# Performance work log

Hardware: AMD Instinct MI355X
Metric: run time of the kernel (lower is better)

Reference implementation:

```python
import jax, jax.numpy as jnp
import numpy as np

B, T, E = 4, 2048, 1024
H, D = 8, 128  # num_query_heads, head_dimension (single shared KV head -> MQA)


def sinusoidal_pe(length, dim, dtype=jnp.float32):
    """Standard additive sinusoidal PE table of shape (length, dim)."""
    pos = jnp.arange(length, dtype=jnp.float32)[:, None]            # (L, 1)
    inv_freq = jnp.exp(-jnp.log(jnp.float32(10000.0)) * (jnp.arange(0, dim, 2, dtype=jnp.float32) / dim))
    ang = pos * inv_freq[None, :]                                    # (L, dim//2)
    pe = jnp.zeros((length, dim), dtype=jnp.float32)
    pe = pe.at[:, 0::2].set(jnp.sin(ang)).at[:, 1::2].set(jnp.cos(ang))
    return pe.astype(dtype)


def setup_inputs() -> dict:
    key = jax.random.key(0)
    kx, kq, kk, kv, ko = jax.random.split(key, 5)
    s = 0.02  # weight init scale
    return {
        "x": jax.random.normal(kx, (B, T, E), dtype=jnp.float32),
        "Wq": jax.random.normal(kq, (H * D, E), dtype=jnp.float32) * s,
        "Wk": jax.random.normal(kk, (D, E), dtype=jnp.float32) * s,
        "Wv": jax.random.normal(kv, (D, E), dtype=jnp.float32) * s,
        "Wo": jax.random.normal(ko, (E, H * D), dtype=jnp.float32) * s,
    }


def reference(x, Wq, Wk, Wv, Wo):
    Bv, Tv, Ev = x.shape
    scale = 1.0 / jnp.sqrt(jnp.float32(D)).astype(x.dtype)

    q = (x @ Wq.T).reshape(Bv, Tv, H, D)        # (B, T, H, D)
    k = (x @ Wk.T).reshape(Bv, Tv, 1, D)        # (B, T, 1, D) single KV head
    v = (x @ Wv.T).reshape(Bv, Tv, 1, D)

    # positional_embedding applied along axis -2 (as in (.., seq, dim) layout):
    # for k (B,T,1,D) the -2 axis has length 1 -> adds pe[0];
    # for q after permute (B,H,T,D) the -2 axis is T -> full table.
    k = k + sinusoidal_pe(1, D, k.dtype)        # broadcast over (B, T)

    q = jnp.transpose(q, (0, 2, 1, 3))          # (B, H, T, D)
    k1 = k[:, :, 0, :]                          # (B, T, D) shared KV head
    v1 = v[:, :, 0, :]                          # (B, T, D)

    q = q + sinusoidal_pe(Tv, D, q.dtype)[None, None]

    # MQA SDPA: broadcast single K/V head across H query heads
    scores = jnp.einsum("bhtd,bsd->bhts", q, k1) * scale   # (B, H, T, T)
    causal = jnp.tril(jnp.ones((Tv, Tv), dtype=bool))
    scores = jnp.where(causal[None, None], scores, jnp.finfo(scores.dtype).min)
    probs = jax.nn.softmax(scores, axis=-1)
    attn = jnp.einsum("bhts,bsd->bhtd", probs, v1)          # (B, H, T, D)

    out = jnp.transpose(attn, (0, 2, 1, 3)).reshape(Bv, Tv, H * D)
    return out @ Wo.T                                        # (B, T, E)
```

## Files before the change

kernel.cpp:

```cpp
#include <hip/hip_runtime.h>
#include <hip/hip_bf16.h>
#include <cstdint>
#include <cstddef>

#define B_ 4
#define T_ 2048
#define E_ 1024
#define H_ 8
#define D_ 128

typedef unsigned short u16;
typedef __bf16 bf16x8 __attribute__((ext_vector_type(8)));
typedef float f32x4 __attribute__((ext_vector_type(4)));

#define MFMA16(a, b, c) __builtin_amdgcn_mfma_f32_16x16x32_bf16((a), (b), (c), 0, 0, 0)

#if defined(__has_builtin)
#if __has_builtin(__builtin_amdgcn_global_load_lds)
#define HAVE_GLL 1
#endif
#endif

__device__ __forceinline__ void gload_lds16(const u16* g, u16* l) {
#ifdef HAVE_GLL
  __builtin_amdgcn_global_load_lds(
      (const __attribute__((address_space(1))) void*)g,
      (__attribute__((address_space(3))) void*)l, 16, 0, 0);
#else
  int lane = threadIdx.x & 63;
  *(uint4*)(l + lane * 8) = *(const uint4*)(g);
#endif
}

__device__ __forceinline__ u16 f2bf(float f) {
  union { float f; uint32_t u; } a; a.f = f;
  uint32_t u = a.u;
  uint32_t r = (u + 0x7fffu + ((u >> 16) & 1u)) >> 16;
  return (u16)r;
}

__device__ __forceinline__ uint32_t pkbf(float lo, float hi) {
  uint32_t r;
  asm volatile("v_cvt_pk_bf16_f32 %0, %1, %2" : "=v"(r) : "v"(lo), "v"(hi));
  return r;
}

__device__ __forceinline__ void cvt4(const float* __restrict__ s, u16* __restrict__ d, int i4) {
  float4 v = *(const float4*)(s + (size_t)i4 * 4);
  uint2 o;
  o.x = (uint32_t)f2bf(v.x) | ((uint32_t)f2bf(v.y) << 16);
  o.y = (uint32_t)f2bf(v.z) | ((uint32_t)f2bf(v.w) << 16);
  *(uint2*)(d + (size_t)i4 * 4) = o;
}

__global__ __launch_bounds__(256) void prep_kernel(
    const float* __restrict__ x,  const float* __restrict__ Wq,
    const float* __restrict__ Wk, const float* __restrict__ Wv,
    const float* __restrict__ Wo,
    u16* __restrict__ xbf, u16* __restrict__ Wcat, u16* __restrict__ Wobf,
    float* __restrict__ pe)
{
  int id = blockIdx.x * 256 + threadIdx.x;
  if (id < 2097152) { cvt4(x, xbf, id); return; }
  id -= 2097152;
  if (id < 262144) { cvt4(Wq, Wcat, id); return; }
  id -= 262144;
  if (id < 32768) { cvt4(Wk, Wcat + 1048576, id); return; }
  id -= 32768;
  if (id < 32768) { cvt4(Wv, Wcat + 1179648, id); return; }
  id -= 32768;
  if (id < 262144) { cvt4(Wo, Wobf, id); return; }
  id -= 262144;
  int t = id >> 6, i = id & 63;
  float f = expf(-logf(10000.0f) * (float)i / 64.0f);
  float ang = (float)t * f;
  pe[t * 128 + 2 * i]     = sinf(ang);
  pe[t * 128 + 2 * i + 1] = cosf(ang);
}

template<int MODE>
__global__ __launch_bounds__(256) void gemm_nt(
    const u16* __restrict__ A, const u16* __restrict__ Bm,
    u16* __restrict__ Qb, u16* __restrict__ Kb, u16* __restrict__ VTb,
    const float* __restrict__ pe, float* __restrict__ Cout, int K)
{
  __shared__ u16 Al[128 * 32];
  __shared__ u16 Bl[128 * 32];
  const int t = threadIdx.x;
  const int l = t & 63, w = t >> 6;
  const int wr = w >> 1, wc = w & 1;
  const int bm = blockIdx.x * 128, bn = blockIdx.y * 128;
  const int lr = l & 15, lg = l >> 4;

  const int srow = w * 32 + (l >> 2);
  const int scol = (l & 3) * 8;
  const u16* gA0 = A + (size_t)(bm + srow) * K + scol;
  const u16* gB0 = Bm + (size_t)(bn + srow) * K + scol;
  u16* lA0 = &Al[(w * 32) * 32];
  u16* lA1 = &Al[(w * 32 + 16) * 32];
  u16* lB0 = &Bl[(w * 32) * 32];
  u16* lB1 = &Bl[(w * 32 + 16) * 32];
  const size_t r16 = (size_t)16 * K;

  f32x4 acc[4][4] = {};

  for (int k0 = 0; k0 < K; k0 += 32) {
    gload_lds16(gA0 + k0, lA0);
    gload_lds16(gA0 + r16 + k0, lA1);
    gload_lds16(gB0 + k0, lB0);
    gload_lds16(gB0 + r16 + k0, lB1);
    __syncthreads();
    bf16x8 af[4], bfr[4];
    #pragma unroll
    for (int m = 0; m < 4; ++m)
      af[m] = *(const bf16x8*)(&Al[(wr * 64 + m * 16 + lr) * 32 + lg * 8]);
    #pragma unroll
    for (int n = 0; n < 4; ++n)
      bfr[n] = *(const bf16x8*)(&Bl[(wc * 64 + n * 16 + lr) * 32 + lg * 8]);
    __builtin_amdgcn_s_setprio(1);
    #pragma unroll
    for (int m = 0; m < 4; ++m) {
      #pragma unroll
      for (int n = 0; n < 4; ++n)
        acc[m][n] = MFMA16(af[m], bfr[n], acc[m][n]);
    }
    __builtin_amdgcn_s_setprio(0);
    __syncthreads();
  }

  const float qscale = 0.08838834764831845f;
  #pragma unroll
  for (int m = 0; m < 4; ++m) {
    #pragma unroll
    for (int n = 0; n < 4; ++n) {
      const int gm0 = bm + wr * 64 + m * 16 + lg * 4;
      const int gn = bn + wc * 64 + n * 16 + lr;
      if constexpr (MODE == 0) {
        const int b = gm0 >> 11, tq0 = gm0 & (T_ - 1);
        if (gn < 1024) {
          int hh = gn >> 7, d = gn & 127;
          #pragma unroll
          for (int r = 0; r < 4; ++r)
            Qb[(((size_t)(b * H_ + hh) * T_ + tq0 + r) << 7) + d] =
                f2bf((acc[m][n][r] + pe[((tq0 + r) << 7) + d]) * qscale);
        } else if (gn < 1152) {
          int d = gn - 1024;
          #pragma unroll
          for (int r = 0; r < 4; ++r)
            Kb[((size_t)(gm0 + r) << 7) + d] = f2bf(acc[m][n][r] + (float)(d & 1));
        } else {
          int d = gn - 1152;
          uint2 pk;
          pk.x = pkbf(acc[m][n][0], acc[m][n][1]);
          pk.y = pkbf(acc[m][n][2], acc[m][n][3]);
          *(uint2*)(VTb + ((size_t)(b * 128 + d) << 11) + tq0) = pk;
        }
      } else {
        #pragma unroll
        for (int r = 0; r < 4; ++r)
          Cout[(size_t)(gm0 + r) * 1024 + gn] = acc[m][n][r];
      }
    }
  }
}

__global__ __launch_bounds__(512) void attn_kernel(
    const u16* __restrict__ Qb, const u16* __restrict__ Kb,
    const u16* __restrict__ VTg, u16* __restrict__ Ob)
{
  __shared__ u16 Kl[128 * 136];
  __shared__ u16 VTl[128 * 136];
  __shared__ u16 Pl[8 * 16 * 136];
  const int t = threadIdx.x;
  const int l = t & 63, w = t >> 6;
  const int lr = l & 15, lg = l >> 4;
  const int p = blockIdx.x, b = blockIdx.y;
  const int h = w;
  const int q0A = p * 16, q0B = (127 - p) * 16;
  const int ntA = (q0A + 16 + 127) >> 7, ntB = (q0B + 16 + 127) >> 7;

  const u16* qbA = Qb + (((size_t)(b * H_ + h) * T_ + q0A + lr) << 7);
  const u16* qbB = Qb + (((size_t)(b * H_ + h) * T_ + q0B + lr) << 7);
  bf16x8 qfA[4], qfB[4];
  #pragma unroll
  for (int kc = 0; kc < 4; ++kc) {
    qfA[kc] = *(const bf16x8*)(qbA + kc * 32 + lg * 8);
    qfB[kc] = *(const bf16x8*)(qbB + kc * 32 + lg * 8);
  }

  float mA = -3e38f, mB = -3e38f, lA = 0.f, lB = 0.f;
  f32x4 oA[8] = {}, oB[8] = {};
  u16* pw = &Pl[w * 16 * 136];

  auto process = [&](f32x4 (&s)[8], float& m, float& lsum, f32x4 (&o)[8],
                     int q0F, int kt, bool masked) {
    float pv[32];
    float pm = -3e38f;
    if (masked) {
      const int qv = q0F + lr;
      #pragma unroll
      for (int kvf = 0; kvf < 8; ++kvf) {
        #pragma unroll
        for (int r = 0; r < 4; ++r) {
          int kv = kt * 128 + kvf * 16 + lg * 4 + r;
          float sv = (kv <= qv) ? s[kvf][r] : -3e38f;
          pv[kvf * 4 + r] = sv;
          pm = fmaxf(pm, sv);
        }
      }
    } else {
      #pragma unroll
      for (int kvf = 0; kvf < 8; ++kvf) {
        #pragma unroll
        for (int r = 0; r < 4; ++r) {
          float sv = s[kvf][r];
          pv[kvf * 4 + r] = sv;
          pm = fmaxf(pm, sv);
        }
      }
    }
    pm = fmaxf(pm, __shfl_xor(pm, 16));
    pm = fmaxf(pm, __shfl_xor(pm, 32));
    float mn;
    if (__all(pm <= m + 8.0f)) {
      mn = m;
    } else {
      mn = fmaxf(m, pm);
      float corr = __expf(m - mn);
      lsum *= corr;
      #pragma unroll
      for (int df = 0; df < 8; ++df) {
        #pragma unroll
        for (int r = 0; r < 4; ++r) o[df][r] *= corr;
      }
      m = mn;
    }
    float ps = 0.f;
    #pragma unroll
    for (int i = 0; i < 32; ++i) {
      pv[i] = __expf(pv[i] - mn);
      ps += pv[i];
    }
    ps += __shfl_xor(ps, 16);
    ps += __shfl_xor(ps, 32);
    lsum += ps;
    #pragma unroll
    for (int kvf = 0; kvf < 8; ++kvf) {
      uint2 pk;
      pk.x = pkbf(pv[kvf * 4 + 0], pv[kvf * 4 + 1]);
      pk.y = pkbf(pv[kvf * 4 + 2], pv[kvf * 4 + 3]);
      *(uint2*)(&pw[lr * 136 + kvf * 16 + lg * 4]) = pk;
    }
    __builtin_amdgcn_s_setprio(1);
    #pragma unroll
    for (int kc = 0; kc < 4; ++kc) {
      bf16x8 pf = *(const bf16x8*)(&pw[lr * 136 + kc * 32 + lg * 8]);
      #pragma unroll
      for (int df = 0; df < 8; ++df) {
        bf16x8 vf = *(const bf16x8*)(&VTl[(df * 16 + lr) * 136 + kc * 32 + lg * 8]);
        o[df] = MFMA16(vf, pf, o[df]);
      }
    }
    __builtin_amdgcn_s_setprio(0);
  };

  for (int kt = 0; kt < ntB; ++kt) {
    #pragma unroll
    for (int it = 0; it < 4; ++it) {
      int cc = it * 512 + t;
      int row = cc >> 4, u = cc & 15;
      *(uint4*)(&Kl[row * 136 + u * 8]) =
          *(const uint4*)(Kb + ((size_t)(b * T_ + kt * 128 + row) << 7) + u * 8);
      *(uint4*)(&VTl[row * 136 + u * 8]) =
          *(const uint4*)(VTg + ((size_t)(b * 128 + row) << 11) + kt * 128 + u * 8);
    }
    __syncthreads();

    const bool actA = kt < ntA;
    f32x4 sA[8] = {}, sB[8] = {};
    __builtin_amdgcn_s_setprio(1);
    #pragma unroll
    for (int kvf = 0; kvf < 8; ++kvf) {
      bf16x8 kf[4];
      #pragma unroll
      for (int kc = 0; kc < 4; ++kc)
        kf[kc] = *(const bf16x8*)(&Kl[(kvf * 16 + lr) * 136 + kc * 32 + lg * 8]);
      #pragma unroll
      for (int kc = 0; kc < 4; ++kc)
        sB[kvf] = MFMA16(kf[kc], qfB[kc], sB[kvf]);
      if (actA) {
        #pragma unroll
        for (int kc = 0; kc < 4; ++kc)
          sA[kvf] = MFMA16(kf[kc], qfA[kc], sA[kvf]);
      }
    }
    __builtin_amdgcn_s_setprio(0);
    process(sB, mB, lB, oB, q0B, kt, kt * 128 + 127 > q0B);
    if (actA) process(sA, mA, lA, oA, q0A, kt, kt * 128 + 127 > q0A);
    __syncthreads();
  }

  float rA = 1.0f / lA, rB = 1.0f / lB;
  #pragma unroll
  for (int df = 0; df < 8; ++df) {
    uint2 pk;
    pk.x = pkbf(oB[df][0] * rB, oB[df][1] * rB);
    pk.y = pkbf(oB[df][2] * rB, oB[df][3] * rB);
    *(uint2*)(Ob + ((size_t)(b * T_ + q0B + lr) << 10) + h * 128 + df * 16 + lg * 4) = pk;
    pk.x = pkbf(oA[df][0] * rA, oA[df][1] * rA);
    pk.y = pkbf(oA[df][2] * rA, oA[df][3] * rA);
    *(uint2*)(Ob + ((size_t)(b * T_ + q0A + lr) << 10) + h * 128 + df * 16 + lg * 4) = pk;
  }
}

extern "C" void kernel_launch(void* const* d_in, const int* in_sizes, int n_in,
                              void* d_out, int out_size, void* d_ws, size_t ws_size,
                              hipStream_t stream) {
  const float* x  = (const float*)d_in[0];
  const float* Wq = (const float*)d_in[1];
  const float* Wk = (const float*)d_in[2];
  const float* Wv = (const float*)d_in[3];
  const float* Wo = (const float*)d_in[4];

  char* ws = (char*)d_ws;
  size_t off = 0;
  auto alloc = [&](size_t bytes) {
    char* p = ws + off;
    off += (bytes + 255) & ~(size_t)255;
    return p;
  };
  u16*   xbf  = (u16*)  alloc(8388608ull * 2);
  u16*   Wcat = (u16*)  alloc(1310720ull * 2);
  u16*   Wobf = (u16*)  alloc(1048576ull * 2);
  float* pe   = (float*)alloc(262144ull * 4);
  u16*   Qbuf = (u16*)  alloc(8388608ull * 2);
  u16*   Kbuf = (u16*)  alloc(1048576ull * 2);
  u16*   VTbuf= (u16*)  alloc(1048576ull * 2);
  u16*   Abuf = (u16*)  alloc(8388608ull * 2);

  prep_kernel<<<11008, 256, 0, stream>>>(x, Wq, Wk, Wv, Wo, xbf, Wcat, Wobf, pe);

  gemm_nt<0><<<dim3(64, 10), 256, 0, stream>>>(xbf, Wcat, Qbuf, Kbuf, VTbuf, pe, nullptr, 1024);
  attn_kernel<<<dim3(64, 4), 512, 0, stream>>>(Qbuf, Kbuf, VTbuf, Abuf);
  gemm_nt<1><<<dim3(64, 8), 256, 0, stream>>>(Abuf, Wobf, nullptr, nullptr, nullptr, nullptr,
                                              (float*)d_out, 1024);
}
```

Baseline: 153.5 us.

## Interleave softmax for both query tiles, use exp2 with log2e-folded scale

The two query tiles (A and B) handled by each wave now share one softmax and PV pass: separate P buffers in LDS let the max, exp and sum steps for both tiles interleave. The PV loop loads each V fragment once and feeds it to both accumulators. The Q scale now includes log2(e), so exp2f replaces __expf and the rescale threshold becomes 11.5 in base 2. This cuts redundant V loads from LDS and gives the scheduler more independent work, at the cost of more LDS and higher register pressure.

```diff
diff --git a/kernel.cpp b/kernel.cpp
--- a/kernel.cpp
+++ b/kernel.cpp
@@ -2,6 +2,7 @@
 #include <hip/hip_bf16.h>
 #include <cstdint>
 #include <cstddef>
+#include <cmath>
 
 #define B_ 4
 #define T_ 2048
@@ -128,7 +129,7 @@
     __syncthreads();
   }
 
-  const float qscale = 0.08838834764831845f;
+  const float qscale = 0.12752869468f;
   #pragma unroll
   for (int m = 0; m < 4; ++m) {
     #pragma unroll
@@ -170,7 +171,8 @@
 {
   __shared__ u16 Kl[128 * 136];
   __shared__ u16 VTl[128 * 136];
-  __shared__ u16 Pl[8 * 16 * 136];
+  __shared__ u16 PlB[8 * 16 * 136];
+  __shared__ u16 PlA[8 * 16 * 136];
   const int t = threadIdx.x;
   const int l = t & 63, w = t >> 6;
   const int lr = l & 15, lg = l >> 4;
@@ -190,79 +192,8 @@
 
   float mA = -3e38f, mB = -3e38f, lA = 0.f, lB = 0.f;
   f32x4 oA[8] = {}, oB[8] = {};
-  u16* pw = &Pl[w * 16 * 136];
-
-  auto process = [&](f32x4 (&s)[8], float& m, float& lsum, f32x4 (&o)[8],
-                     int q0F, int kt, bool masked) {
-    float pv[32];
-    float pm = -3e38f;
-    if (masked) {
-      const int qv = q0F + lr;
-      #pragma unroll
-      for (int kvf = 0; kvf < 8; ++kvf) {
-        #pragma unroll
-        for (int r = 0; r < 4; ++r) {
-          int kv = kt * 128 + kvf * 16 + lg * 4 + r;
-          float sv = (kv <= qv) ? s[kvf][r] : -3e38f;
-          pv[kvf * 4 + r] = sv;
-          pm = fmaxf(pm, sv);
-        }
-      }
-    } else {
-      #pragma unroll
-      for (int kvf = 0; kvf < 8; ++kvf) {
-        #pragma unroll
-        for (int r = 0; r < 4; ++r) {
-          float sv = s[kvf][r];
-          pv[kvf * 4 + r] = sv;
-          pm = fmaxf(pm, sv);
-        }
-      }
-    }
-    pm = fmaxf(pm, __shfl_xor(pm, 16));
-    pm = fmaxf(pm, __shfl_xor(pm, 32));
-    float mn;
-    if (__all(pm <= m + 8.0f)) {
-      mn = m;
-    } else {
-      mn = fmaxf(m, pm);
-      float corr = __expf(m - mn);
-      lsum *= corr;
-      #pragma unroll
-      for (int df = 0; df < 8; ++df) {
-        #pragma unroll
-        for (int r = 0; r < 4; ++r) o[df][r] *= corr;
-      }
-      m = mn;
-    }
-    float ps = 0.f;
-    #pragma unroll
-    for (int i = 0; i < 32; ++i) {
-      pv[i] = __expf(pv[i] - mn);
-      ps += pv[i];
-    }
-    ps += __shfl_xor(ps, 16);
-    ps += __shfl_xor(ps, 32);
-    lsum += ps;
-    #pragma unroll
-    for (int kvf = 0; kvf < 8; ++kvf) {
-      uint2 pk;
-      pk.x = pkbf(pv[kvf * 4 + 0], pv[kvf * 4 + 1]);
-      pk.y = pkbf(pv[kvf * 4 + 2], pv[kvf * 4 + 3]);
-      *(uint2*)(&pw[lr * 136 + kvf * 16 + lg * 4]) = pk;
-    }
-    __builtin_amdgcn_s_setprio(1);
-    #pragma unroll
-    for (int kc = 0; kc < 4; ++kc) {
-      bf16x8 pf = *(const bf16x8*)(&pw[lr * 136 + kc * 32 + lg * 8]);
-      #pragma unroll
-      for (int df = 0; df < 8; ++df) {
-        bf16x8 vf = *(const bf16x8*)(&VTl[(df * 16 + lr) * 136 + kc * 32 + lg * 8]);
-        o[df] = MFMA16(vf, pf, o[df]);
-      }
-    }
-    __builtin_amdgcn_s_setprio(0);
-  };
+  u16* pwB = &PlB[w * 16 * 136];
+  u16* pwA = &PlA[w * 16 * 136];
 
   for (int kt = 0; kt < ntB; ++kt) {
     #pragma unroll
@@ -295,8 +226,132 @@
       }
     }
     __builtin_amdgcn_s_setprio(0);
-    process(sB, mB, lB, oB, q0B, kt, kt * 128 + 127 > q0B);
-    if (actA) process(sA, mA, lA, oA, q0A, kt, kt * 128 + 127 > q0A);
+
+    const bool mskB = kt * 128 + 127 > q0B;
+    const bool mskA = kt * 128 + 127 > q0A;
+    const int qvB = q0B + lr, qvA = q0A + lr;
+    const int kvb0 = kt * 128 + lg * 4;
+
+    float pmB = -3e38f, pmA = -3e38f;
+    if (mskB) {
+      #pragma unroll
+      for (int kvf = 0; kvf < 8; ++kvf) {
+        #pragma unroll
+        for (int r = 0; r < 4; ++r)
+          if (kvb0 + kvf * 16 + r <= qvB) pmB = fmaxf(pmB, sB[kvf][r]);
+      }
+    } else {
+      #pragma unroll
+      for (int kvf = 0; kvf < 8; ++kvf) {
+        #pragma unroll
+        for (int r = 0; r < 4; ++r) pmB = fmaxf(pmB, sB[kvf][r]);
+      }
+    }
+    if (actA) {
+      if (mskA) {
+        #pragma unroll
+        for (int kvf = 0; kvf < 8; ++kvf) {
+          #pragma unroll
+          for (int r = 0; r < 4; ++r)
+            if (kvb0 + kvf * 16 + r <= qvA) pmA = fmaxf(pmA, sA[kvf][r]);
+        }
+      } else {
+        #pragma unroll
+        for (int kvf = 0; kvf < 8; ++kvf) {
+          #pragma unroll
+          for (int r = 0; r < 4; ++r) pmA = fmaxf(pmA, sA[kvf][r]);
+        }
+      }
+    }
+    pmB = fmaxf(pmB, __shfl_xor(pmB, 16));
+    pmB = fmaxf(pmB, __shfl_xor(pmB, 32));
+    if (actA) {
+      pmA = fmaxf(pmA, __shfl_xor(pmA, 16));
+      pmA = fmaxf(pmA, __shfl_xor(pmA, 32));
+    }
+
+    float mnB;
+    if (__all(pmB <= mB + 11.5f)) {
+      mnB = mB;
+    } else {
+      mnB = fmaxf(mB, pmB);
+      float c = exp2f(mB - mnB);
+      lB *= c;
+      #pragma unroll
+      for (int df = 0; df < 8; ++df) {
+        #pragma unroll
+        for (int r = 0; r < 4; ++r) oB[df][r] *= c;
+      }
+      mB = mnB;
+    }
+    float mnA = mA;
+    if (actA && !__all(pmA <= mA + 11.5f)) {
+      mnA = fmaxf(mA, pmA);
+      float c = exp2f(mA - mnA);
+      lA *= c;
+      #pragma unroll
+      for (int df = 0; df < 8; ++df) {
+        #pragma unroll
+        for (int r = 0; r < 4; ++r) oA[df][r] *= c;
+      }
+      mA = mnA;
+    }
+
+    float psB = 0.f;
+    #pragma unroll
+    for (int kvf = 0; kvf < 8; ++kvf) {
+      float e[4];
+      #pragma unroll
+      for (int r = 0; r < 4; ++r) {
+        float sv = (!mskB || (kvb0 + kvf * 16 + r <= qvB)) ? sB[kvf][r] : -3e38f;
+        e[r] = exp2f(sv - mnB);
+        psB += e[r];
+      }
+      uint2 pk;
+      pk.x = pkbf(e[0], e[1]);
+      pk.y = pkbf(e[2], e[3]);
+      *(uint2*)(&pwB[lr * 136 + kvf * 16 + lg * 4]) = pk;
+    }
+    float psA = 0.f;
+    if (actA) {
+      #pragma unroll
+      for (int kvf = 0; kvf < 8; ++kvf) {
+        float e[4];
+        #pragma unroll
+        for (int r = 0; r < 4; ++r) {
+          float sv = (!mskA || (kvb0 + kvf * 16 + r <= qvA)) ? sA[kvf][r] : -3e38f;
+          e[r] = exp2f(sv - mnA);
+          psA += e[r];
+        }
+        uint2 pk;
+        pk.x = pkbf(e[0], e[1]);
+        pk.y = pkbf(e[2], e[3]);
+        *(uint2*)(&pwA[lr * 136 + kvf * 16 + lg * 4]) = pk;
+      }
+    }
+    psB += __shfl_xor(psB, 16);
+    psB += __shfl_xor(psB, 32);
+    lB += psB;
+    if (actA) {
+      psA += __shfl_xor(psA, 16);
+      psA += __shfl_xor(psA, 32);
+      lA += psA;
+    }
+
+    __builtin_amdgcn_s_setprio(1);
+    #pragma unroll
+    for (int kc = 0; kc < 4; ++kc) {
+      bf16x8 pfB = *(const bf16x8*)(&pwB[lr * 136 + kc * 32 + lg * 8]);
+      bf16x8 pfA;
+      if (actA) pfA = *(const bf16x8*)(&pwA[lr * 136 + kc * 32 + lg * 8]);
+      #pragma unroll
+      for (int df = 0; df < 8; ++df) {
+        bf16x8 vf = *(const bf16x8*)(&VTl[(df * 16 + lr) * 136 + kc * 32 + lg * 8]);
+        oB[df] = MFMA16(vf, pfB, oB[df]);
+        if (actA) oA[df] = MFMA16(vf, pfA, oA[df]);
+      }
+    }
+    __builtin_amdgcn_s_setprio(0);
     __syncthreads();
   }
 
```

Result: slower. 334.3 us (+117.8%).
